# Optimization experiments

Hardware: AMD Instinct MI355X
Metric: run time of the kernel (lower is better)

The kernel has to match this reference:

```python
import jax, jax.numpy as jnp
import numpy as np


def setup_inputs() -> dict:
    key = jax.random.key(0)
    k1, k2 = jax.random.split(key)
    B, L = 16384, 4096
    v = jax.random.normal(k1, (B, L), dtype=jnp.float32)
    z = jax.random.normal(k2, (B, L), dtype=jnp.float32)
    return {"v": v, "z": z}


def reference(v, z):
    # Householder reflection: z_new = z - 2 * v (v . z) / ||v||^2
    # Algebraically identical to the original's bmm(v v^T, z) formulation,
    # but avoids materializing the [B, L, L] outer product.
    vz = jnp.sum(v * z, axis=1, keepdims=True)       # [B, 1]
    norm_sq = jnp.sum(v * v, axis=1, keepdims=True)  # [B, 1]
    return z - 2.0 * v * (vz / norm_sq)
```

## Files before the change

kernel.cpp:

```cpp
#include <hip/hip_runtime.h>


#define L 4096
#define WAVES_PER_BLOCK 4
#define BLOCK (WAVES_PER_BLOCK * 64)
#define F4 (L / (64 * 4))

typedef float f32x4 __attribute__((ext_vector_type(4)));

__global__ __launch_bounds__(BLOCK, 1) void hh_kernel(
    const float* __restrict__ v,
    const float* __restrict__ z,
    float* __restrict__ out)
{
    const int wave = threadIdx.x >> 6;
    const int lane = threadIdx.x & 63;
    const long long row  = (long long)blockIdx.x * WAVES_PER_BLOCK + wave;
    const long long base = row * (long long)L;

    const f32x4* v4 = reinterpret_cast<const f32x4*>(v + base);
    const f32x4* z4 = reinterpret_cast<const f32x4*>(z + base);
    f32x4*       o4 = reinterpret_cast<f32x4*>(out + base);

    f32x4 vr[F4];
    f32x4 zr[F4];

#pragma unroll
    for (int i = 0; i < F4; ++i) {
        vr[i] = v4[lane + i * 64];
        zr[i] = z4[lane + i * 64];
    }

    f32x4 dotv = {0.f, 0.f, 0.f, 0.f};
    f32x4 nsqv = {0.f, 0.f, 0.f, 0.f};
#pragma unroll
    for (int i = 0; i < F4; ++i) {
        dotv += vr[i] * zr[i];
        nsqv += vr[i] * vr[i];
    }
    float dot = dotv.x + dotv.y + dotv.z + dotv.w;
    float nsq = nsqv.x + nsqv.y + nsqv.z + nsqv.w;

#pragma unroll
    for (int off = 32; off > 0; off >>= 1) {
        dot += __shfl_xor(dot, off, 64);
        nsq += __shfl_xor(nsq, off, 64);
    }

    const float s = -2.0f * dot / nsq;

#pragma unroll
    for (int i = 0; i < F4; ++i) {
        f32x4 o = zr[i] + s * vr[i];
        __builtin_nontemporal_store(o, &o4[lane + i * 64]);
    }
}

extern "C" void kernel_launch(void* const* d_in, const int* in_sizes, int n_in,
                              void* d_out, int out_size, void* d_ws, size_t ws_size,
                              hipStream_t stream) {
    const float* v = (const float*)d_in[0];
    const float* z = (const float*)d_in[1];
    float* out = (float*)d_out;

    const int B = in_sizes[0] / L;
    hh_kernel<<<B / WAVES_PER_BLOCK, BLOCK, 0, stream>>>(v, z, out);
}
```

Before: 577.9 us.

## Persistent single-wave blocks with double-buffered global-to-LDS async row prefetch

Replaces the one-row-per-wave grid with 512 persistent single-wave blocks that loop over rows. Each block prefetches the next row's v and z straight into LDS with global_load_lds while it computes the current row, so memory loads overlap with compute and the output stores. The cost is 64KB of LDS per block, which limits occupancy, and only one wave per block is in flight to hide latency. It also depends on hand-written vmcnt waits being correct.

```diff
diff --git a/kernel.cpp b/kernel.cpp
--- a/kernel.cpp
+++ b/kernel.cpp
@@ -1,58 +1,89 @@
 #include <hip/hip_runtime.h>
+#include <cstdint>
 
 
 #define L 4096
-#define WAVES_PER_BLOCK 4
-#define BLOCK (WAVES_PER_BLOCK * 64)
-#define F4 (L / (64 * 4))
+#define NBLK 512
+#define SEGS 16
 
 typedef float f32x4 __attribute__((ext_vector_type(4)));
 
-__global__ __launch_bounds__(BLOCK, 1) void hh_kernel(
+__global__ __launch_bounds__(64, 1) void hh_kernel(
     const float* __restrict__ v,
     const float* __restrict__ z,
-    float* __restrict__ out)
+    float* __restrict__ out, int B)
 {
-    const int wave = threadIdx.x >> 6;
+    __shared__ float vbuf[2][L];
+    __shared__ float zbuf[2][L];
+
     const int lane = threadIdx.x & 63;
-    const long long row  = (long long)blockIdx.x * WAVES_PER_BLOCK + wave;
-    const long long base = row * (long long)L;
+    const int bid  = blockIdx.x;
+    const int nit = (B - bid + NBLK - 1) / NBLK;
+    if (nit <= 0) return;
 
-    const f32x4* v4 = reinterpret_cast<const f32x4*>(v + base);
-    const f32x4* z4 = reinterpret_cast<const f32x4*>(z + base);
-    f32x4*       o4 = reinterpret_cast<f32x4*>(out + base);
+    auto stage = [&](int buf, int row) {
+        const float* vsrc = v + (long long)row * L + lane * 4;
+        const float* zsrc = z + (long long)row * L + lane * 4;
+#pragma unroll
+        for (int s = 0; s < SEGS; ++s)
+            __builtin_amdgcn_global_load_lds(
+                (const __attribute__((address_space(1))) uint32_t*)(vsrc + s * 256),
+                (__attribute__((address_space(3))) uint32_t*)&vbuf[buf][s * 256],
+                16, 0, 0);
+#pragma unroll
+        for (int s = 0; s < SEGS; ++s)
+            __builtin_amdgcn_global_load_lds(
+                (const __attribute__((address_space(1))) uint32_t*)(zsrc + s * 256),
+                (__attribute__((address_space(3))) uint32_t*)&zbuf[buf][s * 256],
+                16, 0, 0);
+    };
 
-    f32x4 vr[F4];
-    f32x4 zr[F4];
+    stage(0, bid);
+
+    for (int it = 0; it < nit; ++it) {
+        const int  cur  = it & 1;
+        const bool more = (it + 1 < nit);
+
+        if (more) stage(cur ^ 1, bid + (it + 1) * NBLK);
+
+        if (more) asm volatile("s_waitcnt vmcnt(32)" ::: "memory");
+        else      asm volatile("s_waitcnt vmcnt(0)"  ::: "memory");
+
+        const f32x4* vb = (const f32x4*)vbuf[cur];
+        const f32x4* zb = (const f32x4*)zbuf[cur];
+
+        f32x4 d0 = {0,0,0,0}, d1 = {0,0,0,0}, d2 = {0,0,0,0}, d3 = {0,0,0,0};
+        f32x4 n0 = {0,0,0,0}, n1 = {0,0,0,0}, n2 = {0,0,0,0}, n3 = {0,0,0,0};
+#pragma unroll
+        for (int i = 0; i < 16; i += 4) {
+            f32x4 a0 = vb[lane + (i+0)*64], b0 = zb[lane + (i+0)*64];
+            f32x4 a1 = vb[lane + (i+1)*64], b1 = zb[lane + (i+1)*64];
+            f32x4 a2 = vb[lane + (i+2)*64], b2 = zb[lane + (i+2)*64];
+            f32x4 a3 = vb[lane + (i+3)*64], b3 = zb[lane + (i+3)*64];
+            d0 += a0*b0; n0 += a0*a0;
+            d1 += a1*b1; n1 += a1*a1;
+            d2 += a2*b2; n2 += a2*a2;
+            d3 += a3*b3; n3 += a3*a3;
+        }
+        f32x4 dv = (d0 + d1) + (d2 + d3);
+        f32x4 nv = (n0 + n1) + (n2 + n3);
+        float dot = dv.x + dv.y + dv.z + dv.w;
+        float nsq = nv.x + nv.y + nv.z + nv.w;
 
 #pragma unroll
-    for (int i = 0; i < F4; ++i) {
-        vr[i] = v4[lane + i * 64];
-        zr[i] = z4[lane + i * 64];
-    }
+        for (int off = 32; off > 0; off >>= 1) {
+            dot += __shfl_xor(dot, off, 64);
+            nsq += __shfl_xor(nsq, off, 64);
+        }
+        const float s = -2.0f * dot / nsq;
 
-    f32x4 dotv = {0.f, 0.f, 0.f, 0.f};
-    f32x4 nsqv = {0.f, 0.f, 0.f, 0.f};
+        f32x4* o4 = (f32x4*)(out + (long long)(bid + it * NBLK) * L);
 #pragma unroll
-    for (int i = 0; i < F4; ++i) {
-        dotv += vr[i] * zr[i];
-        nsqv += vr[i] * vr[i];
-    }
-    float dot = dotv.x + dotv.y + dotv.z + dotv.w;
-    float nsq = nsqv.x + nsqv.y + nsqv.z + nsqv.w;
-
-#pragma unroll
-    for (int off = 32; off > 0; off >>= 1) {
-        dot += __shfl_xor(dot, off, 64);
-        nsq += __shfl_xor(nsq, off, 64);
-    }
-
-    const float s = -2.0f * dot / nsq;
-
-#pragma unroll
-    for (int i = 0; i < F4; ++i) {
-        f32x4 o = zr[i] + s * vr[i];
-        __builtin_nontemporal_store(o, &o4[lane + i * 64]);
+        for (int i = 0; i < 16; ++i) {
+            f32x4 vv = vb[lane + i*64];
+            f32x4 zz = zb[lane + i*64];
+            __builtin_nontemporal_store(zz + s * vv, o4 + lane + i*64);
+        }
     }
 }
 
@@ -64,5 +95,5 @@
     float* out = (float*)d_out;
 
     const int B = in_sizes[0] / L;
-    hh_kernel<<<B / WAVES_PER_BLOCK, BLOCK, 0, stream>>>(v, z, out);
+    hh_kernel<<<NBLK, 64, 0, stream>>>(v, z, out, B);
 }
```

After: 588.3 us. Within noise of the previous version (+1.8%).
